# Performance work log

Hardware: AMD Instinct MI355X
Metric: run time of the kernel (lower is better)

The kernel has to match this reference:

```python
import jax, jax.numpy as jnp
import numpy as np

BS, N, E = 16, 1024, 262144
IN_DIM, HID, OUT, NREL, NBASES = 3072, 512, 128, 8, 4
N_LAYERS = 3


def setup_inputs() -> dict:
    key = jax.random.key(0)
    ks = jax.random.split(key, 10)
    tot = BS * N
    return {
        "h": jax.random.normal(ks[0], (BS, N, IN_DIM), jnp.float32),
        "src": jax.random.randint(ks[1], (E,), 0, tot, jnp.int32),
        "dst": jax.random.randint(ks[2], (E,), 0, tot, jnp.int32),
        "r": jax.random.randint(ks[3], (E,), 0, NREL, jnp.int32),
        "norm": jax.random.uniform(ks[4], (E,), jnp.float32),
        "W_elmo": jax.random.normal(ks[5], (IN_DIM, 256), jnp.float32) * 0.02,
        "b_elmo": jnp.zeros((256,), jnp.float32),
        "comp": jax.random.normal(ks[6], (NREL, NBASES), jnp.float32),
        "V": jax.random.normal(ks[7], (NBASES, HID, HID), jnp.float32) * 0.04,
        "b_gcn": jnp.zeros((HID,), jnp.float32),
        "W_out": jax.random.normal(ks[8], (HID, OUT), jnp.float32) * 0.04,
        "b_out": jnp.zeros((OUT,), jnp.float32),
    }


def reference(h, src, dst, r, norm, W_elmo, b_elmo, comp, V, b_gcn, W_out, b_out):
    bs, n, _ = h.shape
    tot = bs * n
    # elmo_fnn + relu, then concat with zeros -> gnn_h_dim = 512
    x = jax.nn.relu(h @ W_elmo + b_elmo)                 # [bs, N, 256]
    x = jnp.concatenate([x, jnp.zeros_like(x)], axis=-1)  # [bs, N, 512]
    x = x.reshape(tot, HID)                               # flattened batched-graph nodes

    coef = comp[r]  # [E, NBASES] per-edge relation coefficients (basis decomposition)
    nb = V.shape[0]
    for _ in range(N_LAYERS):  # shared RelGraphConv applied repeatedly
        hs = x[src]  # [E, HID] gather source node features per edge
        # message m_e = h_src @ (sum_b comp[r_e, b] * V_b); loop over small fixed basis count
        msg = coef[:, 0:1] * (hs @ V[0])
        for b in range(1, nb):
            msg = msg + coef[:, b:b + 1] * (hs @ V[b])
        msg = msg * norm[:, None]  # per-edge norm weighting
        x = jax.ops.segment_sum(msg, dst, num_segments=tot)  # scatter-aggregate to dst
        x = jax.nn.relu(x + b_gcn)  # bias + activation (no self-loop, dropout=0)

    x = x.reshape(bs, n, HID).mean(axis=1)  # mean over nodes per graph
    logits = x @ W_out + b_out
    return jax.nn.softmax(logits, axis=-1)
```

## Files before the change

### kernel.cpp

```cpp
#include <hip/hip_runtime.h>

typedef unsigned short u16;
typedef unsigned int   u32;
typedef u16   u16x4 __attribute__((ext_vector_type(4)));
typedef u16   u16x8 __attribute__((ext_vector_type(8)));
typedef short s16x8 __attribute__((ext_vector_type(8)));
typedef u32   u32x4 __attribute__((ext_vector_type(4)));
typedef int   s32x4 __attribute__((ext_vector_type(4)));
typedef float f32x4 __attribute__((ext_vector_type(4)));

__device__ __forceinline__ float bf2f(u16 u) {
    u32 x = ((u32)u) << 16;
    return __builtin_bit_cast(float, x);
}
__device__ __forceinline__ u16 f2bf(float f) {
    u32 u = __builtin_bit_cast(u32, f);
    u32 r = u + 0x7FFFu + ((u >> 16) & 1u);
    return (u16)(r >> 16);
}
__device__ __forceinline__ u32 cvtpk(float a, float b) {
    u32 r;
    asm("v_cvt_pk_bf16_f32 %0, %1, %2" : "=v"(r) : "v"(a), "v"(b));
    return r;
}

__device__ __forceinline__ void gload16(const void* g, void* lds) {
    __builtin_amdgcn_global_load_lds((const __attribute__((address_space(1))) void*)g,
                                     (__attribute__((address_space(3))) void*)lds, 16, 0, 0);
}

#define TOT   16384
#define HID   512
#define NRELS 8
#define EDGES 262144
#define INDIM 3072
#define NOUT  128
#define NGRAPH 16
#define NODESPER 1024
#define EKSPLIT 4

#define OFF_XB     ((size_t)0)
#define OFF_Y      (OFF_XB + 16777216)
#define OFF_WCT    (OFF_Y + 134217728)
#define OFF_WET    (OFF_WCT + 4194304)
#define OFF_CNT    (OFF_WET + 1572864)
#define OFF_ROWPTR (OFF_CNT + 65536)
#define OFF_CURSOR (OFF_ROWPTR + 65552)
#define OFF_EPK    (OFF_CURSOR + 65536)
#define OFF_ENORM  (OFF_EPK + 1048576)
#define OFF_PART   (OFF_ENORM + 1048576)

__global__ __launch_bounds__(256) void k_prep_wcat(const float* __restrict__ comp,
                                                   const float* __restrict__ V,
                                                   u16* __restrict__ WcatT) {
    __shared__ float tile[64][65];
    const int r = blockIdx.z, k0 = blockIdx.x * 64, n0 = blockIdx.y * 64;
    const float c0 = comp[r * 4], c1 = comp[r * 4 + 1], c2 = comp[r * 4 + 2], c3 = comp[r * 4 + 3];
    const int tn = threadIdx.x & 63;
    const int tk = threadIdx.x >> 6;
#pragma unroll
    for (int i = 0; i < 16; ++i) {
        int k = tk + i * 4;
        const float* vp = V + (size_t)(k0 + k) * 512 + n0 + tn;
        tile[k][tn] = c0 * vp[0] + c1 * vp[262144] + c2 * vp[2 * 262144] + c3 * vp[3 * 262144];
    }
    __syncthreads();
    const int kk = threadIdx.x & 63;
#pragma unroll
    for (int i = 0; i < 16; ++i) {
        int n = (threadIdx.x >> 6) + i * 4;
        WcatT[((size_t)(r * 512 + n0 + n) << 9) + k0 + kk] = f2bf(tile[kk][n]);
    }
}

__global__ __launch_bounds__(256) void k_prep_welmo(const float* __restrict__ W,
                                                    u16* __restrict__ WT) {
    __shared__ float tile[64][65];
    const int k0 = blockIdx.x * 64, n0 = blockIdx.y * 64;
    const int tn = threadIdx.x & 63;
    const int tk = threadIdx.x >> 6;
#pragma unroll
    for (int i = 0; i < 16; ++i) {
        int k = tk + i * 4;
        tile[k][tn] = W[(size_t)(k0 + k) * 256 + n0 + tn];
    }
    __syncthreads();
    const int kk = threadIdx.x & 63;
#pragma unroll
    for (int i = 0; i < 16; ++i) {
        int n = (threadIdx.x >> 6) + i * 4;
        WT[(size_t)(n0 + n) * 3072 + k0 + kk] = f2bf(tile[kk][n]);
    }
}

__global__ __launch_bounds__(256) void k_hist(const int* __restrict__ dst, int* __restrict__ cnt) {
    int e = blockIdx.x * 256 + threadIdx.x;
    atomicAdd(&cnt[dst[e]], 1);
}

__global__ __launch_bounds__(1024) void k_scan(const int* __restrict__ cnt,
                                               int* __restrict__ rowptr,
                                               int* __restrict__ cursor) {
    __shared__ int part[1024];
    int t = threadIdx.x;
    int loc[16];
    int s = 0;
    int base = t * 16;
#pragma unroll
    for (int i = 0; i < 16; ++i) { loc[i] = s; s += cnt[base + i]; }
    part[t] = s;
    __syncthreads();
    for (int off = 1; off < 1024; off <<= 1) {
        int v = (t >= off) ? part[t - off] : 0;
        __syncthreads();
        part[t] += v;
        __syncthreads();
    }
    int excl = (t == 0) ? 0 : part[t - 1];
#pragma unroll
    for (int i = 0; i < 16; ++i) {
        int v = excl + loc[i];
        rowptr[base + i] = v;
        cursor[base + i] = v;
    }
    if (t == 1023) rowptr[TOT] = part[1023];
}

__global__ __launch_bounds__(256) void k_scatter(const int* __restrict__ src,
                                                 const int* __restrict__ dst,
                                                 const int* __restrict__ rel,
                                                 const float* __restrict__ norm,
                                                 int* __restrict__ cursor,
                                                 int* __restrict__ epk,
                                                 float* __restrict__ enorm) {
    int e = blockIdx.x * 256 + threadIdx.x;
    int d = dst[e];
    int pos = atomicAdd(&cursor[d], 1);
    epk[pos] = (src[e] << 3) | rel[e];
    enorm[pos] = norm[e];
}

__global__ __launch_bounds__(256, 2) void k_gemm(const u16* __restrict__ A,
                                                 const u16* __restrict__ BT,
                                                 u16* __restrict__ C,
                                                 int K, int lda, int ldb, int ldc) {
    __shared__ __align__(16) u16 As[128 * 64];
    __shared__ __align__(16) u16 Bs[256 * 64];

    const int t = threadIdx.x;
    const int lin = blockIdx.y * 128 + blockIdx.x;
    const int xcd = lin & 7, q = lin >> 3;
    const int tileM = (xcd * 16 + (q >> 4)) * 128;
    const int tileN = (q & 15) * 256;

    const int w = t >> 6, l = t & 63;
    const int wr = w >> 1, wc = w & 1;
    const int lo = l & 15, hi = l >> 4;

    const int srow8 = l >> 3;
    const int scol = ((l & 7) ^ srow8) * 8;

    f32x4 acc[4][8];
#pragma unroll
    for (int m = 0; m < 4; ++m)
#pragma unroll
        for (int n = 0; n < 8; ++n) acc[m][n] = f32x4{0.f, 0.f, 0.f, 0.f};

    for (int k0 = 0; k0 < K; k0 += 64) {
#pragma unroll
        for (int i = 0; i < 4; ++i) {
            const int rowblk = (w * 4 + i) * 8;
            gload16(A + (size_t)(tileM + rowblk + srow8) * lda + k0 + scol, &As[rowblk * 64]);
        }
#pragma unroll
        for (int i = 0; i < 8; ++i) {
            const int rowblk = (w * 8 + i) * 8;
            gload16(BT + (size_t)(tileN + rowblk + srow8) * ldb + k0 + scol, &Bs[rowblk * 64]);
        }
        __syncthreads();

#pragma unroll
        for (int kk = 0; kk < 2; ++kk) {
            s16x8 af[4], bf[8];
#pragma unroll
            for (int m = 0; m < 4; ++m) {
                int row = wr * 64 + m * 16 + lo;
                int boff = (row * 128 + kk * 64 + hi * 16) ^ ((row & 7) << 4);
                af[m] = *(const s16x8*)((const char*)As + boff);
            }
#pragma unroll
            for (int n = 0; n < 8; ++n) {
                int row = wc * 128 + n * 16 + lo;
                int boff = (row * 128 + kk * 64 + hi * 16) ^ ((row & 7) << 4);
                bf[n] = *(const s16x8*)((const char*)Bs + boff);
            }
#pragma unroll
            for (int m = 0; m < 4; ++m)
#pragma unroll
                for (int n = 0; n < 8; ++n)
                    acc[m][n] = __builtin_amdgcn_mfma_f32_16x16x32_bf16(
                        af[m], bf[n], acc[m][n], 0, 0, 0);
        }
        __syncthreads();
    }

#pragma unroll
    for (int m = 0; m < 4; ++m)
#pragma unroll
        for (int n = 0; n < 8; ++n) {
            int col = tileN + wc * 128 + n * 16 + lo;
#pragma unroll
            for (int j = 0; j < 4; ++j) {
                int row = tileM + wr * 64 + m * 16 + hi * 4 + j;
                C[(size_t)row * ldc + col] = f2bf(acc[m][n][j]);
            }
        }
}

__global__ __launch_bounds__(256, 2) void k_gemm_elmo(const float* __restrict__ A,
                                                      const u16* __restrict__ BT,
                                                      float* __restrict__ Cp) {
    __shared__ __align__(16) float As[128 * 64];
    __shared__ __align__(16) u16   Bs[256 * 64];

    const int t = threadIdx.x;
    const int tileM = blockIdx.x * 128;
    const int kz = blockIdx.y;
    const int kbeg = kz * (INDIM / EKSPLIT);

    const int w = t >> 6, l = t & 63;
    const int wr = w >> 1, wc = w & 1;
    const int lo = l & 15, hi = l >> 4;

    const int ar = l >> 4;
    const int br = l >> 3;
    const int bcol = ((l & 7) ^ br) * 8;

    f32x4 acc[4][8];
#pragma unroll
    for (int m = 0; m < 4; ++m)
#pragma unroll
        for (int n = 0; n < 8; ++n) acc[m][n] = f32x4{0.f, 0.f, 0.f, 0.f};

    for (int ks = 0; ks < 12; ++ks) {
        const int k0 = kbeg + ks * 64;
#pragma unroll
        for (int i = 0; i < 8; ++i) {
            const int RA = (w * 8 + i) * 4;
            const int ca = (l & 15) ^ ((RA & 15) + ar);
            gload16(A + (size_t)(tileM + RA + ar) * INDIM + k0 + ca * 4, &As[RA * 64]);
            const int RB = (w * 8 + i) * 8;
            gload16(BT + (size_t)(RB + br) * INDIM + k0 + bcol, &Bs[RB * 64]);
        }
        __syncthreads();

#pragma unroll
        for (int kk = 0; kk < 2; ++kk) {
            s16x8 afr[4], bfr[8];
#pragma unroll
            for (int m = 0; m < 4; ++m) {
                int ra = wr * 64 + m * 16 + lo;
                int x0 = kk * 8 + hi * 2;
                const char* base = (const char*)As + ra * 256;
                f32x4 p = *(const f32x4*)(base + (((x0) ^ (ra & 15)) << 4));
                f32x4 q = *(const f32x4*)(base + (((x0 + 1) ^ (ra & 15)) << 4));
                u32x4 pk = {cvtpk(p[0], p[1]), cvtpk(p[2], p[3]),
                            cvtpk(q[0], q[1]), cvtpk(q[2], q[3])};
                afr[m] = __builtin_bit_cast(s16x8, pk);
            }
#pragma unroll
            for (int n = 0; n < 8; ++n) {
                int rb = wc * 128 + n * 16 + lo;
                int boff = (rb * 128 + kk * 64 + hi * 16) ^ ((rb & 7) << 4);
                bfr[n] = *(const s16x8*)((const char*)Bs + boff);
            }
#pragma unroll
            for (int m = 0; m < 4; ++m)
#pragma unroll
                for (int n = 0; n < 8; ++n)
                    acc[m][n] = __builtin_amdgcn_mfma_f32_16x16x32_bf16(
                        afr[m], bfr[n], acc[m][n], 0, 0, 0);
        }
        __syncthreads();
    }

    float* cp = Cp + (size_t)kz * TOT * 256;
#pragma unroll
    for (int m = 0; m < 4; ++m)
#pragma unroll
        for (int n = 0; n < 8; ++n) {
            int col = wc * 128 + n * 16 + lo;
#pragma unroll
            for (int j = 0; j < 4; ++j) {
                int row = tileM + wr * 64 + m * 16 + hi * 4 + j;
                cp[(size_t)row * 256 + col] = acc[m][n][j];
            }
        }
}

__global__ __launch_bounds__(256) void k_elmo_reduce(const float* __restrict__ Cp,
                                                     const float* __restrict__ bias,
                                                     u16* __restrict__ xb) {
    int idx = blockIdx.x * 256 + threadIdx.x;
    int row = idx >> 6;
    int c4 = (idx & 63) * 4;
    f32x4 s = *(const f32x4*)(Cp + (size_t)row * 256 + c4);
#pragma unroll
    for (int p = 1; p < EKSPLIT; ++p)
        s += *(const f32x4*)(Cp + (size_t)p * TOT * 256 + (size_t)row * 256 + c4);
    f32x4 bv = *(const f32x4*)(bias + c4);
    u16x4 o;
#pragma unroll
    for (int j = 0; j < 4; ++j) o[j] = f2bf(fmaxf(s[j] + bv[j], 0.f));
    *(u16x4*)(xb + (size_t)row * HID + c4) = o;
}

__global__ __launch_bounds__(256, 4) void k_agg(const u16* __restrict__ y,
                                                const int* __restrict__ rowptr,
                                                const int* __restrict__ epk,
                                                const float* __restrict__ enorm,
                                                const float* __restrict__ bgcn,
                                                u16* __restrict__ xout) {
    const int wid = (blockIdx.x * 256 + threadIdx.x) >> 6;
    const int l = threadIdx.x & 63;
    const u32x4* yv = (const u32x4*)y;

    float a[8];
    {
        f32x4 b0 = *(const f32x4*)(bgcn + l * 8);
        f32x4 b1 = *(const f32x4*)(bgcn + l * 8 + 4);
#pragma unroll
        for (int j = 0; j < 4; ++j) { a[j] = b0[j]; a[j + 4] = b1[j]; }
    }

#define ACC1(ee, nq)                                                          \
    {                                                                         \
        u32x4 v_ = yv[(((size_t)((ee) >> 3)) << 9) + (((ee) & 7) << 6) + l];  \
        _Pragma("unroll") for (int j = 0; j < 4; ++j) {                       \
            a[2 * j]     = fmaf((nq), bf2f((u16)v_[j]), a[2 * j]);            \
            a[2 * j + 1] = fmaf((nq), bf2f((u16)(v_[j] >> 16)), a[2 * j + 1]);\
        }                                                                     \
    }

    const int beg = rowptr[wid], end = rowptr[wid + 1];
    int p = beg;
    const int pal = min(end, (beg + 3) & ~3);
    for (; p < pal; ++p) ACC1(epk[p], enorm[p]);

    for (; p + 16 <= end; p += 16) {
        s32x4 e[4];
        f32x4 nn[4];
#pragma unroll
        for (int q4 = 0; q4 < 4; ++q4) {
            e[q4]  = *(const s32x4*)(epk + p + 4 * q4);
            nn[q4] = *(const f32x4*)(enorm + p + 4 * q4);
        }
        u32x4 v[16];
#pragma unroll
        for (int q = 0; q < 16; ++q) {
            int ee = e[q >> 2][q & 3];
            v[q] = yv[(((size_t)(ee >> 3)) << 9) + ((ee & 7) << 6) + l];
        }
#pragma unroll
        for (int q = 0; q < 16; ++q) {
            float nq = nn[q >> 2][q & 3];
#pragma unroll
            for (int j = 0; j < 4; ++j) {
                a[2 * j]     = fmaf(nq, bf2f((u16)v[q][j]), a[2 * j]);
                a[2 * j + 1] = fmaf(nq, bf2f((u16)(v[q][j] >> 16)), a[2 * j + 1]);
            }
        }
    }
    for (; p + 4 <= end; p += 4) {
        s32x4 e4  = *(const s32x4*)(epk + p);
        f32x4 n4  = *(const f32x4*)(enorm + p);
        u32x4 v[4];
#pragma unroll
        for (int q = 0; q < 4; ++q) {
            int ee = e4[q];
            v[q] = yv[(((size_t)(ee >> 3)) << 9) + ((ee & 7) << 6) + l];
        }
#pragma unroll
        for (int q = 0; q < 4; ++q) {
            float nq = n4[q];
#pragma unroll
            for (int j = 0; j < 4; ++j) {
                a[2 * j]     = fmaf(nq, bf2f((u16)v[q][j]), a[2 * j]);
                a[2 * j + 1] = fmaf(nq, bf2f((u16)(v[q][j] >> 16)), a[2 * j + 1]);
            }
        }
    }
    for (; p < end; ++p) ACC1(epk[p], enorm[p]);
#undef ACC1

    u16x8 o;
#pragma unroll
    for (int j = 0; j < 8; ++j) o[j] = f2bf(fmaxf(a[j], 0.f));
    *(u16x8*)(xout + ((size_t)wid << 9) + l * 8) = o;
}

__global__ __launch_bounds__(512) void k_mean1(const u16* __restrict__ xb,
                                               float* __restrict__ part) {
    int g = blockIdx.x >> 4, chunk = blockIdx.x & 15, t = threadIdx.x;
    const u16* base = xb + ((size_t)g * NODESPER + chunk * 64) * HID;
    float s = 0.f;
    for (int n = 0; n < 64; ++n) s += bf2f(base[(size_t)n * HID + t]);
    part[(size_t)blockIdx.x * HID + t] = s;
}

__global__ __launch_bounds__(512) void k_final2(const float* __restrict__ part,
                                                const float* __restrict__ W_out,
                                                const float* __restrict__ b_out,
                                                float* __restrict__ out) {
    int g = blockIdx.x, t = threadIdx.x;
    __shared__ float mean_s[512];
    __shared__ float lg[128];
    __shared__ float red[128];
    float s = 0.f;
#pragma unroll
    for (int c = 0; c < 16; ++c) s += part[((size_t)g * 16 + c) * HID + t];
    mean_s[t] = s * (1.0f / (float)NODESPER);
    __syncthreads();
    if (t < NOUT) {
        float a = b_out[t];
        for (int k = 0; k < HID; ++k) a = fmaf(mean_s[k], W_out[(size_t)k * NOUT + t], a);
        lg[t] = a;
        red[t] = a;
    }
    __syncthreads();
    for (int off = 64; off > 0; off >>= 1) {
        if (t < off) red[t] = fmaxf(red[t], red[t + off]);
        __syncthreads();
    }
    float mx = red[0];
    __syncthreads();
    if (t < NOUT) { float e = expf(lg[t] - mx); lg[t] = e; red[t] = e; }
    __syncthreads();
    for (int off = 64; off > 0; off >>= 1) {
        if (t < off) red[t] += red[t + off];
        __syncthreads();
    }
    if (t < NOUT) out[(size_t)g * NOUT + t] = lg[t] / red[0];
}

extern "C" void kernel_launch(void* const* d_in, const int* in_sizes, int n_in,
                              void* d_out, int out_size, void* d_ws, size_t ws_size,
                              hipStream_t stream) {
    const float* h      = (const float*)d_in[0];
    const int*   src    = (const int*)d_in[1];
    const int*   dst    = (const int*)d_in[2];
    const int*   rel    = (const int*)d_in[3];
    const float* norm   = (const float*)d_in[4];
    const float* W_elmo = (const float*)d_in[5];
    const float* b_elmo = (const float*)d_in[6];
    const float* comp   = (const float*)d_in[7];
    const float* V      = (const float*)d_in[8];
    const float* b_gcn  = (const float*)d_in[9];
    const float* W_out  = (const float*)d_in[10];
    const float* b_out  = (const float*)d_in[11];
    float* out = (float*)d_out;

    char* ws = (char*)d_ws;
    u16*   xb     = (u16*)(ws + OFF_XB);
    u16*   y      = (u16*)(ws + OFF_Y);
    float* elmoP  = (float*)(ws + OFF_Y);
    u16*   wcatT  = (u16*)(ws + OFF_WCT);
    u16*   welmoT = (u16*)(ws + OFF_WET);
    int*   cnt    = (int*)(ws + OFF_CNT);
    int*   rowptr = (int*)(ws + OFF_ROWPTR);
    int*   cursor = (int*)(ws + OFF_CURSOR);
    int*   epk    = (int*)(ws + OFF_EPK);
    float* enorm  = (float*)(ws + OFF_ENORM);
    float* part   = (float*)(ws + OFF_PART);

    hipMemsetAsync(xb, 0, (size_t)TOT * HID * 2, stream);
    hipMemsetAsync(cnt, 0, (size_t)TOT * 4, stream);

    k_prep_wcat<<<dim3(8, 8, 8), 256, 0, stream>>>(comp, V, wcatT);
    k_prep_welmo<<<dim3(48, 4), 256, 0, stream>>>(W_elmo, welmoT);

    k_hist<<<EDGES / 256, 256, 0, stream>>>(dst, cnt);
    k_scan<<<1, 1024, 0, stream>>>(cnt, rowptr, cursor);
    k_scatter<<<EDGES / 256, 256, 0, stream>>>(src, dst, rel, norm, cursor, epk, enorm);

    k_gemm_elmo<<<dim3(128, EKSPLIT), 256, 0, stream>>>(h, welmoT, elmoP);
    k_elmo_reduce<<<4096, 256, 0, stream>>>(elmoP, b_elmo, xb);

    for (int L = 0; L < 3; ++L) {
        const int Keff = (L == 0) ? 256 : 512;
        k_gemm<<<dim3(128, 16), 256, 0, stream>>>(xb, wcatT, y, Keff, HID, HID,
                                                  NRELS * HID);
        k_agg<<<TOT / 4, 256, 0, stream>>>(y, rowptr, epk, enorm, b_gcn, xb);
    }

    k_mean1<<<NGRAPH * 16, 512, 0, stream>>>(xb, part);
    k_final2<<<NGRAPH, 512, 0, stream>>>(part, W_out, b_out, out);
}
```

Measured before the change: 470.3 us.

## Double-buffer 256x256 GEMM tiles, batch wcat relations, vectorize node mean

The per-layer GEMM moves to 256x256 output tiles with 512 threads. It double-buffers the LDS stages and prefetches the tile two steps ahead, with explicit waitcnt, barriers and s_setprio so that global loads overlap MFMA work. The wcat prep now loads the four V bases into shared memory once per tile and writes all eight relations, instead of rereading V once per relation. The mean kernel uses 16-byte vector loads and a shared-memory partial reduction. Together these use much more LDS per block, 128 KB for the GEMM, which may cap occupancy, and the hand-written waitcnt counts must exactly match the number of loads issued.

Measured after the change: 506.6 us. 1.08x slower.

```diff
diff --git a/kernel.cpp b/kernel.cpp
--- a/kernel.cpp
+++ b/kernel.cpp
@@ -53,23 +53,33 @@
 __global__ __launch_bounds__(256) void k_prep_wcat(const float* __restrict__ comp,
                                                    const float* __restrict__ V,
                                                    u16* __restrict__ WcatT) {
-    __shared__ float tile[64][65];
-    const int r = blockIdx.z, k0 = blockIdx.x * 64, n0 = blockIdx.y * 64;
-    const float c0 = comp[r * 4], c1 = comp[r * 4 + 1], c2 = comp[r * 4 + 2], c3 = comp[r * 4 + 3];
+    __shared__ float Vt[4][64][65];
+    const int k0 = blockIdx.x * 64, n0 = blockIdx.y * 64;
     const int tn = threadIdx.x & 63;
     const int tk = threadIdx.x >> 6;
 #pragma unroll
+    for (int b = 0; b < 4; ++b)
+#pragma unroll
+        for (int i = 0; i < 16; ++i) {
+            int k = tk + i * 4;
+            Vt[b][k][tn] = V[((size_t)b << 18) + (size_t)(k0 + k) * 512 + n0 + tn];
+        }
+    __syncthreads();
+    const int kk = threadIdx.x & 63;
+    const int nq = threadIdx.x >> 6;
+    float c[8][4];
+#pragma unroll
+    for (int r = 0; r < 8; ++r)
+#pragma unroll
+        for (int b = 0; b < 4; ++b) c[r][b] = comp[r * 4 + b];
     for (int i = 0; i < 16; ++i) {
-        int k = tk + i * 4;
-        const float* vp = V + (size_t)(k0 + k) * 512 + n0 + tn;
-        tile[k][tn] = c0 * vp[0] + c1 * vp[262144] + c2 * vp[2 * 262144] + c3 * vp[3 * 262144];
-    }
-    __syncthreads();
-    const int kk = threadIdx.x & 63;
-#pragma unroll
-    for (int i = 0; i < 16; ++i) {
-        int n = (threadIdx.x >> 6) + i * 4;
-        WcatT[((size_t)(r * 512 + n0 + n) << 9) + k0 + kk] = f2bf(tile[kk][n]);
+        int n = nq + i * 4;
+        float v0 = Vt[0][kk][n], v1 = Vt[1][kk][n], v2 = Vt[2][kk][n], v3 = Vt[3][kk][n];
+#pragma unroll
+        for (int r = 0; r < 8; ++r) {
+            float s = c[r][0] * v0 + c[r][1] * v1 + c[r][2] * v2 + c[r][3] * v3;
+            WcatT[((size_t)(r * 512 + n0 + n) << 9) + k0 + kk] = f2bf(s);
+        }
     }
 }
 
@@ -140,78 +150,116 @@
     enorm[pos] = norm[e];
 }
 
-__global__ __launch_bounds__(256, 2) void k_gemm(const u16* __restrict__ A,
+__global__ __launch_bounds__(512, 2) void k_gemm(const u16* __restrict__ A,
                                                  const u16* __restrict__ BT,
                                                  u16* __restrict__ C,
                                                  int K, int lda, int ldb, int ldc) {
-    __shared__ __align__(16) u16 As[128 * 64];
-    __shared__ __align__(16) u16 Bs[256 * 64];
+    __shared__ __align__(16) u16 As[2][256 * 64];
+    __shared__ __align__(16) u16 Bs[2][256 * 64];
 
     const int t = threadIdx.x;
-    const int lin = blockIdx.y * 128 + blockIdx.x;
+    const int lin = blockIdx.y * 64 + blockIdx.x;
     const int xcd = lin & 7, q = lin >> 3;
-    const int tileM = (xcd * 16 + (q >> 4)) * 128;
+    const int tileM = (xcd * 8 + (q >> 4)) * 256;
     const int tileN = (q & 15) * 256;
 
     const int w = t >> 6, l = t & 63;
-    const int wr = w >> 1, wc = w & 1;
+    const int wr = w >> 2, wc = w & 3;
     const int lo = l & 15, hi = l >> 4;
 
-    const int srow8 = l >> 3;
-    const int scol = ((l & 7) ^ srow8) * 8;
-
-    f32x4 acc[4][8];
-#pragma unroll
-    for (int m = 0; m < 4; ++m)
-#pragma unroll
-        for (int n = 0; n < 8; ++n) acc[m][n] = f32x4{0.f, 0.f, 0.f, 0.f};
-
-    for (int k0 = 0; k0 < K; k0 += 64) {
-#pragma unroll
-        for (int i = 0; i < 4; ++i) {
-            const int rowblk = (w * 4 + i) * 8;
-            gload16(A + (size_t)(tileM + rowblk + srow8) * lda + k0 + scol, &As[rowblk * 64]);
-        }
-#pragma unroll
-        for (int i = 0; i < 8; ++i) {
-            const int rowblk = (w * 8 + i) * 8;
-            gload16(BT + (size_t)(tileN + rowblk + srow8) * ldb + k0 + scol, &Bs[rowblk * 64]);
-        }
-        __syncthreads();
-
-#pragma unroll
-        for (int kk = 0; kk < 2; ++kk) {
-            s16x8 af[4], bf[8];
-#pragma unroll
-            for (int m = 0; m < 4; ++m) {
-                int row = wr * 64 + m * 16 + lo;
-                int boff = (row * 128 + kk * 64 + hi * 16) ^ ((row & 7) << 4);
-                af[m] = *(const s16x8*)((const char*)As + boff);
-            }
-#pragma unroll
-            for (int n = 0; n < 8; ++n) {
-                int row = wc * 128 + n * 16 + lo;
-                int boff = (row * 128 + kk * 64 + hi * 16) ^ ((row & 7) << 4);
-                bf[n] = *(const s16x8*)((const char*)Bs + boff);
-            }
-#pragma unroll
-            for (int m = 0; m < 4; ++m)
-#pragma unroll
-                for (int n = 0; n < 8; ++n)
-                    acc[m][n] = __builtin_amdgcn_mfma_f32_16x16x32_bf16(
-                        af[m], bf[n], acc[m][n], 0, 0, 0);
-        }
-        __syncthreads();
-    }
-
-#pragma unroll
-    for (int m = 0; m < 4; ++m)
-#pragma unroll
-        for (int n = 0; n < 8; ++n) {
-            int col = tileN + wc * 128 + n * 16 + lo;
+    const int sr = l >> 3;
+    const int sc = ((l & 7) ^ sr) * 8;
+
+    f32x4 acc[8][4];
+#pragma unroll
+    for (int m = 0; m < 8; ++m)
+#pragma unroll
+        for (int n = 0; n < 4; ++n) acc[m][n] = f32x4{0.f, 0.f, 0.f, 0.f};
+
+    const int NT = K >> 6;
+
+#define STG(slot, ks)                                                                    \
+    {                                                                                    \
+        const int k0_ = (ks) * 64;                                                       \
+        _Pragma("unroll") for (int g = 0; g < 4; ++g) {                                  \
+            const int rb = g * 64 + w * 8;                                               \
+            gload16(A + (size_t)(tileM + rb + sr) * lda + k0_ + sc, &As[slot][rb * 64]); \
+        }                                                                                \
+        _Pragma("unroll") for (int g = 0; g < 4; ++g) {                                  \
+            const int rb = g * 64 + w * 8;                                               \
+            gload16(BT + (size_t)(tileN + rb + sr) * ldb + k0_ + sc, &Bs[slot][rb * 64]);\
+        }                                                                                \
+    }
+
+    STG(0, 0);
+    STG(1, 1);
+    asm volatile("s_waitcnt vmcnt(8)" ::: "memory");
+    __builtin_amdgcn_sched_barrier(0);
+    __builtin_amdgcn_s_barrier();
+    __builtin_amdgcn_sched_barrier(0);
+
+    for (int u = 0; u < NT; ++u) {
+        const int slot = u & 1;
+        const char* Ab = (const char*)As[slot];
+        const char* Bb = (const char*)Bs[slot];
+
+        s16x8 a0[8], b0[4], a1[8], b1[4];
+#pragma unroll
+        for (int m = 0; m < 8; ++m) {
+            int row = wr * 128 + m * 16 + lo;
+            a0[m] = *(const s16x8*)(Ab + ((row * 128 + hi * 16) ^ ((row & 7) << 4)));
+        }
+#pragma unroll
+        for (int n = 0; n < 4; ++n) {
+            int row = wc * 64 + n * 16 + lo;
+            b0[n] = *(const s16x8*)(Bb + ((row * 128 + hi * 16) ^ ((row & 7) << 4)));
+        }
+#pragma unroll
+        for (int m = 0; m < 8; ++m)
+#pragma unroll
+            for (int n = 0; n < 4; ++n)
+                acc[m][n] = __builtin_amdgcn_mfma_f32_16x16x32_bf16(a0[m], b0[n],
+                                                                    acc[m][n], 0, 0, 0);
+#pragma unroll
+        for (int m = 0; m < 8; ++m) {
+            int row = wr * 128 + m * 16 + lo;
+            a1[m] = *(const s16x8*)(Ab + ((row * 128 + 64 + hi * 16) ^ ((row & 7) << 4)));
+        }
+#pragma unroll
+        for (int n = 0; n < 4; ++n) {
+            int row = wc * 64 + n * 16 + lo;
+            b1[n] = *(const s16x8*)(Bb + ((row * 128 + 64 + hi * 16) ^ ((row & 7) << 4)));
+        }
+        asm volatile("s_waitcnt lgkmcnt(0)" ::: "memory");
+        __builtin_amdgcn_sched_barrier(0);
+        __builtin_amdgcn_s_barrier();
+        __builtin_amdgcn_sched_barrier(0);
+
+        if (u + 2 < NT) STG(slot, u + 2);
+        __builtin_amdgcn_s_setprio(1);
+#pragma unroll
+        for (int m = 0; m < 8; ++m)
+#pragma unroll
+            for (int n = 0; n < 4; ++n)
+                acc[m][n] = __builtin_amdgcn_mfma_f32_16x16x32_bf16(a1[m], b1[n],
+                                                                    acc[m][n], 0, 0, 0);
+        __builtin_amdgcn_s_setprio(0);
+        if (u + 2 < NT) asm volatile("s_waitcnt vmcnt(8)" ::: "memory");
+        else            asm volatile("s_waitcnt vmcnt(0)" ::: "memory");
+        __builtin_amdgcn_sched_barrier(0);
+        __builtin_amdgcn_s_barrier();
+        __builtin_amdgcn_sched_barrier(0);
+    }
+#undef STG
+
+#pragma unroll
+    for (int m = 0; m < 8; ++m)
+#pragma unroll
+        for (int n = 0; n < 4; ++n) {
+            int col = tileN + wc * 64 + n * 16 + lo;
 #pragma unroll
             for (int j = 0; j < 4; ++j) {
-                int row = tileM + wr * 64 + m * 16 + hi * 4 + j;
+                int row = tileM + wr * 128 + m * 16 + hi * 4 + j;
                 C[(size_t)row * ldc + col] = f2bf(acc[m][n][j]);
             }
         }
@@ -399,13 +447,30 @@
     *(u16x8*)(xout + ((size_t)wid << 9) + l * 8) = o;
 }
 
-__global__ __launch_bounds__(512) void k_mean1(const u16* __restrict__ xb,
+__global__ __launch_bounds__(256) void k_mean1(const u16* __restrict__ xb,
                                                float* __restrict__ part) {
-    int g = blockIdx.x >> 4, chunk = blockIdx.x & 15, t = threadIdx.x;
-    const u16* base = xb + ((size_t)g * NODESPER + chunk * 64) * HID;
-    float s = 0.f;
-    for (int n = 0; n < 64; ++n) s += bf2f(base[(size_t)n * HID + t]);
-    part[(size_t)blockIdx.x * HID + t] = s;
+    __shared__ float red[4][512];
+    const int g = blockIdx.x >> 4, chunk = blockIdx.x & 15;
+    const int fg = threadIdx.x & 63, rg = threadIdx.x >> 6;
+    const u16* base =
+        xb + ((size_t)(g * NODESPER + chunk * 64 + rg * 16)) * HID + fg * 8;
+    float a[8] = {0.f, 0.f, 0.f, 0.f, 0.f, 0.f, 0.f, 0.f};
+    for (int rr = 0; rr < 16; ++rr) {
+        u16x8 v = *(const u16x8*)(base + (size_t)rr * HID);
+#pragma unroll
+        for (int j = 0; j < 8; ++j) a[j] += bf2f(v[j]);
+    }
+#pragma unroll
+    for (int j = 0; j < 8; ++j) red[rg][fg * 8 + j] = a[j];
+    __syncthreads();
+    if (rg == 0) {
+#pragma unroll
+        for (int j = 0; j < 8; ++j) {
+            int f = fg * 8 + j;
+            part[(size_t)blockIdx.x * HID + f] =
+                red[0][f] + red[1][f] + red[2][f] + red[3][f];
+        }
+    }
 }
 
 __global__ __launch_bounds__(512) void k_final2(const float* __restrict__ part,
@@ -476,7 +541,7 @@
     hipMemsetAsync(xb, 0, (size_t)TOT * HID * 2, stream);
     hipMemsetAsync(cnt, 0, (size_t)TOT * 4, stream);
 
-    k_prep_wcat<<<dim3(8, 8, 8), 256, 0, stream>>>(comp, V, wcatT);
+    k_prep_wcat<<<dim3(8, 8), 256, 0, stream>>>(comp, V, wcatT);
     k_prep_welmo<<<dim3(48, 4), 256, 0, stream>>>(W_elmo, welmoT);
 
     k_hist<<<EDGES / 256, 256, 0, stream>>>(dst, cnt);
@@ -488,11 +553,11 @@
 
     for (int L = 0; L < 3; ++L) {
         const int Keff = (L == 0) ? 256 : 512;
-        k_gemm<<<dim3(128, 16), 256, 0, stream>>>(xb, wcatT, y, Keff, HID, HID,
-                                                  NRELS * HID);
+        k_gemm<<<dim3(64, 16), 512, 0, stream>>>(xb, wcatT, y, Keff, HID, HID,
+                                                 NRELS * HID);
         k_agg<<<TOT / 4, 256, 0, stream>>>(y, rowptr, epk, enorm, b_gcn, xb);
     }
 
-    k_mean1<<<NGRAPH * 16, 512, 0, stream>>>(xb, part);
+    k_mean1<<<NGRAPH * 16, 256, 0, stream>>>(xb, part);
     k_final2<<<NGRAPH, 512, 0, stream>>>(part, W_out, b_out, out);
 }
```
